# Optimization experiments

Hardware: AMD Instinct MI355X
Metric: run time of the kernel (lower is better)

## Reference

```python
import jax, jax.numpy as jnp
import numpy as np

CHAN = 128
IN_CHAN = 3
NB_OUT = 10
K = 2  # maxPoolKer


def affine_grid(theta, H, W):
    # theta: [C,2,3] -> grid [C,H,W,2], torch F.affine_grid align_corners=False
    xs = (2.0 * jnp.arange(W, dtype=jnp.float32) + 1.0) / W - 1.0
    ys = (2.0 * jnp.arange(H, dtype=jnp.float32) + 1.0) / H - 1.0
    gx, gy = jnp.meshgrid(xs, ys)  # [H,W]
    base = jnp.stack([gx, gy, jnp.ones_like(gx)], axis=-1)  # [H,W,3]
    return jnp.einsum('crk,hwk->chwr', theta, base)  # [...,0]=x, [...,1]=y


def grid_sample(img, grid):
    # img [M,H,W], grid [M,H,W,2]; bilinear, zeros padding, align_corners=False
    M, H, W = img.shape
    ix = ((grid[..., 0] + 1.0) * W - 1.0) * 0.5
    iy = ((grid[..., 1] + 1.0) * H - 1.0) * 0.5
    x0 = jnp.floor(ix)
    y0 = jnp.floor(iy)
    wx = ix - x0
    wy = iy - y0

    def tap(xi, yi):
        valid = (xi >= 0) & (xi <= W - 1) & (yi >= 0) & (yi <= H - 1)
        xc = jnp.clip(xi, 0, W - 1).astype(jnp.int32)
        yc = jnp.clip(yi, 0, H - 1).astype(jnp.int32)
        v = jax.vmap(lambda im, y, x: im[y, x])(img, yc, xc)
        return jnp.where(valid, v, 0.0)

    v00 = tap(x0, y0)
    v01 = tap(x0 + 1.0, y0)
    v10 = tap(x0, y0 + 1.0)
    v11 = tap(x0 + 1.0, y0 + 1.0)
    return (1.0 - wy) * ((1.0 - wx) * v00 + wx * v01) + wy * ((1.0 - wx) * v10 + wx * v11)


def geom_layer(x, geo, lin, box):
    # x [B,Ci,H,W]; lin [C,Ci]; geo,box [C,2,3]
    B, Ci, H, W = x.shape
    C = lin.shape[0]
    y = jnp.einsum('ci,bihw->bchw', lin, x)  # channel linear combine
    grid = affine_grid(geo, H, W)            # [C,H,W,2], shared across batch
    samp = jax.vmap(lambda yb: grid_sample(yb, grid))(y)  # [B,C,H,W]
    bgrid = affine_grid(box, H, W)
    boxm = grid_sample(jnp.ones((C, H, W), samp.dtype), bgrid)  # BoxPool mask
    return samp * boxm[None]


def maxpool_g(x, k):
    # MaxPool2d_G: depthwise box-filter conv -> argmax -> gather window from padded x
    B, C, H, W = x.shape
    ch, cw = H // k, W // k
    ker = jnp.ones((1, 1, ch, cw), x.dtype) / (ch + cw)
    xr = x.reshape(B * C, 1, H, W)
    conv = jax.lax.conv_general_dilated(
        xr, ker, (1, 1), [(ch // 2, ch // 2), (cw // 2, cw // 2)])
    conv = conv[:, :, :H, :W].reshape(B, C, H * W)
    argm = jnp.argmax(conv, axis=-1)
    r = argm // H  # original code uses origImgSize[0]; assumes square H==W
    c = argm % W
    padH, padW = H + H // k, W + W // k
    top = padH // 2 - H // 2
    left = padW // 2 - W // 2
    padded = jnp.zeros((B, C, padH, padW), x.dtype).at[:, :, top:top + H, left:left + W].set(x)
    r2 = r + H // (2 * k)
    c2 = c + W // (2 * k)
    ri = r2[..., None] + (jnp.arange(ch) - ch // 2)  # [B,C,ch]
    ci = c2[..., None] + (jnp.arange(cw) - cw // 2)  # [B,C,cw]
    gat = jax.vmap(jax.vmap(lambda p, rr, cc: p[rr[:, None], cc[None, :]]))(padded, ri, ci)
    return gat  # [B,C,ch,cw]


def setup_inputs() -> dict:
    key = jax.random.key(0)
    ks = jax.random.split(key, 12)
    eye = jnp.eye(3, dtype=jnp.float32)[:2]  # [2,3]
    x = jax.random.normal(ks[0], (8, IN_CHAN, 64, 64), dtype=jnp.float32)
    geo0 = eye[None] + 0.1 * jax.random.normal(ks[1], (CHAN, 2, 3), dtype=jnp.float32)
    lin0 = jax.random.uniform(ks[2], (CHAN, IN_CHAN), dtype=jnp.float32)
    box0 = eye[None] + 0.1 * jax.random.normal(ks[3], (CHAN, 2, 3), dtype=jnp.float32)
    geos = eye[None, None] + 0.1 * jax.random.normal(ks[4], (3, CHAN, 2, 3), dtype=jnp.float32)
    lins = jax.random.uniform(ks[5], (3, CHAN, CHAN), dtype=jnp.float32)
    boxes = eye[None, None] + 0.1 * jax.random.normal(ks[6], (3, CHAN, 2, 3), dtype=jnp.float32)
    bound = 1.0 / np.sqrt(CHAN)
    dense_w = jax.random.uniform(ks[7], (NB_OUT, CHAN), dtype=jnp.float32, minval=-bound, maxval=bound)
    dense_b = jax.random.uniform(ks[8], (NB_OUT,), dtype=jnp.float32, minval=-bound, maxval=bound)
    return {"x": x, "geo0": geo0, "lin0": lin0, "box0": box0,
            "geos": geos, "lins": lins, "boxes": boxes,
            "dense_w": dense_w, "dense_b": dense_b}


def reference(x, geo0, lin0, box0, geos, lins, boxes, dense_w, dense_b):
    h = geom_layer(x, geo0, lin0, box0)            # inLay: [8,128,64,64]
    h = geom_layer(h, geos[0], lins[0], boxes[0])  # layer 0
    h = maxpool_g(h, K)                            # layer 1 (maxPoolPos=1): [8,128,32,32]
    h = geom_layer(h, geos[1], lins[1], boxes[1])  # layer 2
    h = geom_layer(h, geos[2], lins[2], boxes[2])  # layer 3
    feat = h
    pooled = feat.mean(axis=-1).mean(axis=-1)      # [B,C]
    out = pooled @ dense_w.T + dense_b             # [B,nbOut]
    return out, feat
```

## Files before the change

### kernel.cpp

```cpp
#include <hip/hip_runtime.h>

#define BB 8
#define CC 128

__device__ __forceinline__ float sample_pad(const float* __restrict__ pl, int stride,
                                            float WF, float ix, float iy) {
  ix = fminf(fmaxf(ix, -1.0f), WF);
  iy = fminf(fmaxf(iy, -1.0f), WF);
  float x0f = floorf(ix), y0f = floorf(iy);
  float wx = ix - x0f, wy = iy - y0f;
  int xi = (int)x0f + 1, yi = (int)y0f + 1;
  const float* p0 = pl + yi * stride + xi;
  float v00 = p0[0], v01 = p0[1], v10 = p0[stride], v11 = p0[stride + 1];
  return (1.0f - wy) * ((1.0f - wx) * v00 + wx * v01) +
         wy * ((1.0f - wx) * v10 + wx * v11);
}

__device__ __forceinline__ float box_mask(float bix, float biy, float WM1) {
  float bx0 = floorf(bix), by0 = floorf(biy);
  float bwx = bix - bx0, bwy = biy - by0;
  float mx = (((bx0 >= 0.0f) && (bx0 <= WM1)) ? (1.0f - bwx) : 0.0f) +
             (((bx0 >= -1.0f) && (bx0 <= WM1 - 1.0f)) ? bwx : 0.0f);
  float my = (((by0 >= 0.0f) && (by0 <= WM1)) ? (1.0f - bwy) : 0.0f) +
             (((by0 >= -1.0f) && (by0 <= WM1 - 1.0f)) ? bwy : 0.0f);
  return mx * my;
}

__global__ __launch_bounds__(256) void inlay_sample_kernel(
    const float* __restrict__ x, const float* __restrict__ lin,
    const float* __restrict__ geo, const float* __restrict__ box,
    const float* __restrict__ db, float* __restrict__ out,
    float* __restrict__ head) {
  const int H = 64, W = 64, HW = 4096;
  __shared__ float cp[67 * 68];
  int bc = blockIdx.x;
  int c = bc & (CC - 1);
  int b = bc >> 7;
  int tid = threadIdx.x;
  if (bc == 0 && tid < 80) head[tid] = db[tid % 10];
  const float* xb = x + (size_t)b * 3 * HW;

  float w0 = lin[c * 3 + 0], w1 = lin[c * 3 + 1], w2 = lin[c * 3 + 2];

  if (tid < 68) {
    cp[tid] = 0.0f; cp[65 * 68 + tid] = 0.0f; cp[66 * 68 + tid] = 0.0f;
  } else if (tid < 132) {
    int r = tid - 67;
    cp[r * 68 + 0] = 0.0f; cp[r * 68 + 65] = 0.0f; cp[r * 68 + 66] = 0.0f;
  }

#pragma unroll
  for (int k = 0; k < 4; ++k) {
    int i4 = tid + k * 256;
    int base = i4 * 4;
    float4 f0 = *reinterpret_cast<const float4*>(&xb[base]);
    float4 f1 = *reinterpret_cast<const float4*>(&xb[HW + base]);
    float4 f2 = *reinterpret_cast<const float4*>(&xb[2 * HW + base]);
    int h = i4 >> 4, w = (i4 & 15) * 4;
    float* d = &cp[(h + 1) * 68 + w + 1];
    d[0] = w0 * f0.x + w1 * f1.x + w2 * f2.x;
    d[1] = w0 * f0.y + w1 * f1.y + w2 * f2.y;
    d[2] = w0 * f0.z + w1 * f1.z + w2 * f2.z;
    d[3] = w0 * f0.w + w1 * f1.w + w2 * f2.w;
  }
  __syncthreads();

  const float* g = geo + c * 6;
  const float* bx = box + c * 6;
  float g0 = g[0], g1 = g[1], g2 = g[2], g3 = g[3], g4 = g[4], g5 = g[5];
  float b0 = bx[0], b1 = bx[1], b2 = bx[2], b3 = bx[3], b4 = bx[4], b5 = bx[5];
  float* o = out + ((size_t)b * CC + c) * HW;

#pragma unroll
  for (int k = 0; k < 16; ++k) {
    int px = tid + k * 256;
    int h = px >> 6, w = px & 63;
    float xs = (2.0f * w + 1.0f) / W - 1.0f;
    float ys = (2.0f * h + 1.0f) / H - 1.0f;
    float ix = ((g0 * xs + g1 * ys + g2 + 1.0f) * W - 1.0f) * 0.5f;
    float iy = ((g3 * xs + g4 * ys + g5 + 1.0f) * H - 1.0f) * 0.5f;
    float samp = sample_pad(cp, 68, 64.0f, ix, iy);
    float bix = ((b0 * xs + b1 * ys + b2 + 1.0f) * W - 1.0f) * 0.5f;
    float biy = ((b3 * xs + b4 * ys + b5 + 1.0f) * H - 1.0f) * 0.5f;
    o[px] = samp * box_mask(bix, biy, 63.0f);
  }
}

__global__ __launch_bounds__(256) void gemm64_kernel(
    const float* __restrict__ lin, const float* __restrict__ x,
    float* __restrict__ y, int HW) {
  const int Ci = 128;
  __shared__ __align__(16) float As[16][68];
  __shared__ __align__(16) float Bs[16][64];
  int b = blockIdx.z;
  const float* xb = x + (size_t)b * Ci * HW;
  float* yb = y + (size_t)b * CC * HW;
  int tid = threadIdx.x;
  int tx = tid & 15, ty = tid >> 4;
  int row0 = blockIdx.y * 64;
  int col0 = blockIdx.x * 64;
  int m = tid >> 2, kq = (tid & 3) * 4;
  int kk = tid >> 4, n4 = (tid & 15) * 4;
  float acc[4][4] = {};
  float4 ra = *reinterpret_cast<const float4*>(&lin[(row0 + m) * Ci + kq]);
  float4 rb = *reinterpret_cast<const float4*>(&xb[(size_t)kk * HW + col0 + n4]);
  for (int k0 = 0; k0 < 128; k0 += 16) {
    __syncthreads();
    As[kq + 0][m] = ra.x; As[kq + 1][m] = ra.y; As[kq + 2][m] = ra.z; As[kq + 3][m] = ra.w;
    *reinterpret_cast<float4*>(&Bs[kk][n4]) = rb;
    __syncthreads();
    if (k0 + 16 < 128) {
      ra = *reinterpret_cast<const float4*>(&lin[(row0 + m) * Ci + k0 + 16 + kq]);
      rb = *reinterpret_cast<const float4*>(&xb[(size_t)(k0 + 16 + kk) * HW + col0 + n4]);
    }
#pragma unroll
    for (int kki = 0; kki < 16; ++kki) {
      float4 a4 = *reinterpret_cast<const float4*>(&As[kki][ty * 4]);
      float4 b4 = *reinterpret_cast<const float4*>(&Bs[kki][tx * 4]);
      float a[4] = {a4.x, a4.y, a4.z, a4.w};
      float bv[4] = {b4.x, b4.y, b4.z, b4.w};
#pragma unroll
      for (int i = 0; i < 4; i++)
#pragma unroll
        for (int j = 0; j < 4; j++) acc[i][j] += a[i] * bv[j];
    }
  }
#pragma unroll
  for (int i = 0; i < 4; i++) {
    float* yr = yb + (size_t)(row0 + ty * 4 + i) * HW + col0 + tx * 4;
    *reinterpret_cast<float4*>(yr) = make_float4(acc[i][0], acc[i][1], acc[i][2], acc[i][3]);
  }
}

__global__ __launch_bounds__(1024, 4) void sampmax_kernel(
    const float* __restrict__ y, const float* __restrict__ geo,
    const float* __restrict__ box, float* __restrict__ out) {
  __shared__ __align__(16) float sp[64 * 68];
  __shared__ __align__(16) float arena[64 * 100];
  __shared__ float wv[16];
  __shared__ int wi[16];
  __shared__ int am_s;
  float* pl = arena;
  float* cb = arena;

  int bc = blockIdx.x;
  int c = bc & (CC - 1);
  int tid = threadIdx.x;

  if (tid < 68) {
    pl[tid] = 0.0f; pl[65 * 68 + tid] = 0.0f; pl[66 * 68 + tid] = 0.0f;
  } else if (tid < 132) {
    int r = tid - 67;
    pl[r * 68 + 0] = 0.0f; pl[r * 68 + 65] = 0.0f; pl[r * 68 + 66] = 0.0f;
  }
  {
    const float* plane = y + (size_t)bc * 4096;
    float4 f = *reinterpret_cast<const float4*>(&plane[tid * 4]);
    int h = tid >> 4, w = (tid & 15) * 4;
    float* d = &pl[(h + 1) * 68 + w + 1];
    d[0] = f.x; d[1] = f.y; d[2] = f.z; d[3] = f.w;
  }
  __syncthreads();

  {
    const float* g = geo + c * 6;
    const float* bx = box + c * 6;
    float g0 = g[0], g1 = g[1], g2 = g[2], g3 = g[3], g4 = g[4], g5 = g[5];
    float b0 = bx[0], b1 = bx[1], b2 = bx[2], b3 = bx[3], b4 = bx[4], b5 = bx[5];
#pragma unroll
    for (int k = 0; k < 4; ++k) {
      int px = tid + k * 1024;
      int h = px >> 6, w = px & 63;
      float xs = (2.0f * w + 1.0f) / 64.0f - 1.0f;
      float ys = (2.0f * h + 1.0f) / 64.0f - 1.0f;
      float ix = ((g0 * xs + g1 * ys + g2 + 1.0f) * 64.0f - 1.0f) * 0.5f;
      float iy = ((g3 * xs + g4 * ys + g5 + 1.0f) * 64.0f - 1.0f) * 0.5f;
      float samp = sample_pad(pl, 68, 64.0f, ix, iy);
      float bix = ((b0 * xs + b1 * ys + b2 + 1.0f) * 64.0f - 1.0f) * 0.5f;
      float biy = ((b3 * xs + b4 * ys + b5 + 1.0f) * 64.0f - 1.0f) * 0.5f;
      sp[h * 68 + w] = samp * box_mask(bix, biy, 63.0f);
    }
  }
  __syncthreads();

  if (tid < 256) {
    int strip = tid >> 4, w4 = (tid & 15) * 4;
    int h0 = strip * 4;
    float4 a = make_float4(0.f, 0.f, 0.f, 0.f);
    float4 keep0 = a, keep1 = a, keep2 = a;
#pragma unroll
    for (int j = 0; j < 32; ++j) {
      int r = h0 + j - 16;
      bool valid = (r >= 0) && (r < 64);
      int rc = valid ? r : 0;
      float4 f = *reinterpret_cast<const float4*>(&sp[rc * 68 + w4]);
      f.x = valid ? f.x : 0.0f; f.y = valid ? f.y : 0.0f;
      f.z = valid ? f.z : 0.0f; f.w = valid ? f.w : 0.0f;
      if (j == 0) keep0 = f;
      if (j == 1) keep1 = f;
      if (j == 2) keep2 = f;
      a.x += f.x; a.y += f.y; a.z += f.z; a.w += f.w;
    }
    *reinterpret_cast<float4*>(&cb[(h0 + 0) * 100 + 16 + w4]) = a;
#pragma unroll
    for (int j = 32; j < 35; ++j) {
      int r = h0 + j - 16;
      bool valid = (r < 64);
      int rc = valid ? r : 0;
      float4 f = *reinterpret_cast<const float4*>(&sp[rc * 68 + w4]);
      f.x = valid ? f.x : 0.0f; f.y = valid ? f.y : 0.0f;
      f.z = valid ? f.z : 0.0f; f.w = valid ? f.w : 0.0f;
      float4 kp = (j == 32) ? keep0 : ((j == 33) ? keep1 : keep2);
      a.x += f.x - kp.x; a.y += f.y - kp.y; a.z += f.z - kp.z; a.w += f.w - kp.w;
      *reinterpret_cast<float4*>(&cb[(h0 + j - 31) * 100 + 16 + w4]) = a;
    }
  } else if (tid < 768) {
    int l = tid - 256;
    int row = l >> 3, gq = l & 7;
    int base = row * 100 + ((gq < 4) ? gq * 4 : 80 + (gq - 4) * 4);
    *reinterpret_cast<float4*>(&cb[base]) = make_float4(0.f, 0.f, 0.f, 0.f);
  }
  __syncthreads();

  float best = -3.402823466e+38f;
  int bidx = 0x7fffffff;
  {
    int h = tid >> 4, w4 = (tid & 15) * 4;
    float s0 = 0.f, k0 = 0.f, k1 = 0.f, k2 = 0.f;
#pragma unroll
    for (int q = 0; q < 8; ++q) {
      float4 f = *reinterpret_cast<const float4*>(&cb[h * 100 + w4 + 4 * q]);
      if (q == 0) { k0 = f.x; k1 = f.y; k2 = f.z; }
      s0 += f.x; s0 += f.y; s0 += f.z; s0 += f.w;
    }
    float4 ft = *reinterpret_cast<const float4*>(&cb[h * 100 + w4 + 32]);
    float s1 = s0 - k0 + ft.x;
    float s2 = s1 - k1 + ft.y;
    float s3 = s2 - k2 + ft.z;
    float sv[4] = {s0, s1, s2, s3};
#pragma unroll
    for (int d = 0; d < 4; ++d) {
      int i = (h << 6) + w4 + d;
      if (sv[d] > best) { best = sv[d]; bidx = i; }
    }
  }
#pragma unroll
  for (int off = 32; off > 0; off >>= 1) {
    float v2 = __shfl_down(best, off);
    int i2 = __shfl_down(bidx, off);
    if (v2 > best || (v2 == best && i2 < bidx)) { best = v2; bidx = i2; }
  }
  if ((tid & 63) == 0) { wv[tid >> 6] = best; wi[tid >> 6] = bidx; }
  __syncthreads();
  if (tid == 0) {
    float bv = wv[0]; int bi = wi[0];
#pragma unroll
    for (int k = 1; k < 16; ++k)
      if (wv[k] > bv || (wv[k] == bv && wi[k] < bi)) { bv = wv[k]; bi = wi[k]; }
    am_s = bi;
  }
  __syncthreads();

  int am = am_s;
  int r = am >> 6, cx = am & 63;
  float* o = out + (size_t)bc * 1024;
  {
    int oi = tid >> 5, oj = tid & 31;
    int rr = r + oi - 16, cj = cx + oj - 16;
    bool v = (rr >= 0) && (rr < 64) && (cj >= 0) && (cj < 64);
    int rrc = v ? rr : 0, cjc = v ? cj : 0;
    o[tid] = v ? sp[rrc * 68 + cjc] : 0.0f;
  }
}

template <bool POOL>
__global__ __launch_bounds__(256) void fused32_kernel(
    const float* __restrict__ lin, const float* __restrict__ x,
    const float* __restrict__ geo, const float* __restrict__ box,
    float* __restrict__ out, const float* __restrict__ dw,
    float* __restrict__ head) {
  const int H = 32, W = 32, HW = 1024;
  __shared__ float pls[2][35 * 36];
  __shared__ float wred[8];
  __shared__ float wsum[2];
  int b = blockIdx.x & 7;
  int c0 = (blockIdx.x >> 3) * 2;
  int tid = threadIdx.x;
  const float* xb = x + (size_t)b * 128 * HW;
  const float* l0 = lin + (c0 + 0) * 128;
  const float* l1 = lin + (c0 + 1) * 128;
  int px4 = tid * 4;

  if (tid < 36) {
#pragma unroll
    for (int cch = 0; cch < 2; ++cch) {
      pls[cch][tid] = 0.0f;
      pls[cch][33 * 36 + tid] = 0.0f;
      pls[cch][34 * 36 + tid] = 0.0f;
    }
  } else if (tid < 68) {
    int r = tid - 35;
#pragma unroll
    for (int cch = 0; cch < 2; ++cch) {
      pls[cch][r * 36 + 0] = 0.0f;
      pls[cch][r * 36 + 33] = 0.0f;
      pls[cch][r * 36 + 34] = 0.0f;
      pls[cch][r * 36 + 35] = 0.0f;
    }
  }

  float4 acc0 = make_float4(0.f, 0.f, 0.f, 0.f);
  float4 acc1 = acc0;
#pragma unroll 8
  for (int k = 0; k < 128; ++k) {
    float4 xv = *reinterpret_cast<const float4*>(&xb[(size_t)k * HW + px4]);
    float s0 = l0[k], s1 = l1[k];
    acc0.x += s0 * xv.x; acc0.y += s0 * xv.y; acc0.z += s0 * xv.z; acc0.w += s0 * xv.w;
    acc1.x += s1 * xv.x; acc1.y += s1 * xv.y; acc1.z += s1 * xv.z; acc1.w += s1 * xv.w;
  }
  {
    int h = px4 >> 5, w = px4 & 31;
    float* d0 = &pls[0][(h + 1) * 36 + w + 1];
    d0[0] = acc0.x; d0[1] = acc0.y; d0[2] = acc0.z; d0[3] = acc0.w;
    float* d1 = &pls[1][(h + 1) * 36 + w + 1];
    d1[0] = acc1.x; d1[1] = acc1.y; d1[2] = acc1.z; d1[3] = acc1.w;
  }
  __syncthreads();

  float psum[2] = {0.f, 0.f};
#pragma unroll
  for (int c = 0; c < 2; ++c) {
    const float* g = geo + (c0 + c) * 6;
    const float* bxp = box + (c0 + c) * 6;
    float g0 = g[0], g1 = g[1], g2 = g[2], g3 = g[3], g4 = g[4], g5 = g[5];
    float b0 = bxp[0], b1 = bxp[1], b2 = bxp[2], b3 = bxp[3], b4 = bxp[4], b5 = bxp[5];
    float* o = out + ((size_t)b * CC + c0 + c) * HW;
    const float* pl = pls[c];
#pragma unroll
    for (int k = 0; k < 4; ++k) {
      int px = tid + k * 256;
      int h = px >> 5, w = px & 31;
      float xs = (2.0f * w + 1.0f) / W - 1.0f;
      float ys = (2.0f * h + 1.0f) / H - 1.0f;
      float ix = ((g0 * xs + g1 * ys + g2 + 1.0f) * W - 1.0f) * 0.5f;
      float iy = ((g3 * xs + g4 * ys + g5 + 1.0f) * H - 1.0f) * 0.5f;
      float samp = sample_pad(pl, 36, 32.0f, ix, iy);
      float bix = ((b0 * xs + b1 * ys + b2 + 1.0f) * W - 1.0f) * 0.5f;
      float biy = ((b3 * xs + b4 * ys + b5 + 1.0f) * H - 1.0f) * 0.5f;
      float res = samp * box_mask(bix, biy, 31.0f);
      o[px] = res;
      if (POOL) psum[c] += res;
    }
  }
  if (POOL) {
    int lane = tid & 63, wid = tid >> 6;
#pragma unroll
    for (int c = 0; c < 2; ++c) {
      float r = psum[c];
#pragma unroll
      for (int off = 32; off > 0; off >>= 1) r += __shfl_down(r, off);
      if (lane == 0) wred[c * 4 + wid] = r;
    }
    __syncthreads();
    if (tid < 2) {
      float t = wred[tid * 4] + wred[tid * 4 + 1] + wred[tid * 4 + 2] + wred[tid * 4 + 3];
      wsum[tid] = t * (1.0f / 1024.0f);
    }
    __syncthreads();
    if (tid < 10) {
      float s = wsum[0] * dw[tid * 128 + c0] + wsum[1] * dw[tid * 128 + c0 + 1];
      atomicAdd(&head[b * 10 + tid], s);
    }
  }
}

extern "C" void kernel_launch(void* const* d_in, const int* in_sizes, int n_in,
                              void* d_out, int out_size, void* d_ws, size_t ws_size,
                              hipStream_t stream) {
  const float* x     = (const float*)d_in[0];
  const float* geo0  = (const float*)d_in[1];
  const float* lin0  = (const float*)d_in[2];
  const float* box0  = (const float*)d_in[3];
  const float* geos  = (const float*)d_in[4];
  const float* lins  = (const float*)d_in[5];
  const float* boxes = (const float*)d_in[6];
  const float* dw    = (const float*)d_in[7];
  const float* db    = (const float*)d_in[8];

  float* out  = (float*)d_out;
  float* feat = out + 80;
  float* ws   = (float*)d_ws;
  float* ws0  = ws;
  float* ws1  = ws + 4194304;

  inlay_sample_kernel<<<dim3(BB * CC), 256, 0, stream>>>(x, lin0, geo0, box0, db, ws1, out);
  gemm64_kernel<<<dim3(64, 2, BB), 256, 0, stream>>>(lins, ws1, ws0, 4096);
  sampmax_kernel<<<dim3(BB * CC), 1024, 0, stream>>>(ws0, geos, boxes, ws1);
  fused32_kernel<false><<<dim3(512), 256, 0, stream>>>(lins + 16384, ws1, geos + 768, boxes + 768, ws0, nullptr, nullptr);
  fused32_kernel<true><<<dim3(512), 256, 0, stream>>>(lins + 32768, ws0, geos + 1536, boxes + 1536, feat, dw, out);
}
```

Before: 157.5 us.

## Split 32x32 layers into tiled GEMM plus sampling kernels; shrink sampmax blocks

```diff
diff --git a/kernel.cpp b/kernel.cpp
--- a/kernel.cpp
+++ b/kernel.cpp
@@ -132,13 +132,13 @@
   }
 }
 
-__global__ __launch_bounds__(1024, 4) void sampmax_kernel(
+__global__ __launch_bounds__(256) void sampmax_kernel(
     const float* __restrict__ y, const float* __restrict__ geo,
     const float* __restrict__ box, float* __restrict__ out) {
   __shared__ __align__(16) float sp[64 * 68];
-  __shared__ __align__(16) float arena[64 * 100];
-  __shared__ float wv[16];
-  __shared__ int wi[16];
+  __shared__ __align__(16) float arena[67 * 68];
+  __shared__ float wv[4];
+  __shared__ int wi[4];
   __shared__ int am_s;
   float* pl = arena;
   float* cb = arena;
@@ -155,10 +155,14 @@
   }
   {
     const float* plane = y + (size_t)bc * 4096;
-    float4 f = *reinterpret_cast<const float4*>(&plane[tid * 4]);
-    int h = tid >> 4, w = (tid & 15) * 4;
-    float* d = &pl[(h + 1) * 68 + w + 1];
-    d[0] = f.x; d[1] = f.y; d[2] = f.z; d[3] = f.w;
+#pragma unroll
+    for (int k = 0; k < 4; ++k) {
+      int i4 = tid + k * 256;
+      float4 f = *reinterpret_cast<const float4*>(&plane[i4 * 4]);
+      int h = i4 >> 4, w = (i4 & 15) * 4;
+      float* d = &pl[(h + 1) * 68 + w + 1];
+      d[0] = f.x; d[1] = f.y; d[2] = f.z; d[3] = f.w;
+    }
   }
   __syncthreads();
 
@@ -168,8 +172,8 @@
     float g0 = g[0], g1 = g[1], g2 = g[2], g3 = g[3], g4 = g[4], g5 = g[5];
     float b0 = bx[0], b1 = bx[1], b2 = bx[2], b3 = bx[3], b4 = bx[4], b5 = bx[5];
 #pragma unroll
-    for (int k = 0; k < 4; ++k) {
-      int px = tid + k * 1024;
+    for (int k = 0; k < 16; ++k) {
+      int px = tid + k * 256;
       int h = px >> 6, w = px & 63;
       float xs = (2.0f * w + 1.0f) / 64.0f - 1.0f;
       float ys = (2.0f * h + 1.0f) / 64.0f - 1.0f;
@@ -183,7 +187,7 @@
   }
   __syncthreads();
 
-  if (tid < 256) {
+  {
     int strip = tid >> 4, w4 = (tid & 15) * 4;
     int h0 = strip * 4;
     float4 a = make_float4(0.f, 0.f, 0.f, 0.f);
@@ -201,7 +205,7 @@
       if (j == 2) keep2 = f;
       a.x += f.x; a.y += f.y; a.z += f.z; a.w += f.w;
     }
-    *reinterpret_cast<float4*>(&cb[(h0 + 0) * 100 + 16 + w4]) = a;
+    *reinterpret_cast<float4*>(&cb[(h0 + 0) * 68 + w4]) = a;
 #pragma unroll
     for (int j = 32; j < 35; ++j) {
       int r = h0 + j - 16;
@@ -212,31 +216,40 @@
       f.z = valid ? f.z : 0.0f; f.w = valid ? f.w : 0.0f;
       float4 kp = (j == 32) ? keep0 : ((j == 33) ? keep1 : keep2);
       a.x += f.x - kp.x; a.y += f.y - kp.y; a.z += f.z - kp.z; a.w += f.w - kp.w;
-      *reinterpret_cast<float4*>(&cb[(h0 + j - 31) * 100 + 16 + w4]) = a;
-    }
-  } else if (tid < 768) {
-    int l = tid - 256;
-    int row = l >> 3, gq = l & 7;
-    int base = row * 100 + ((gq < 4) ? gq * 4 : 80 + (gq - 4) * 4);
-    *reinterpret_cast<float4*>(&cb[base]) = make_float4(0.f, 0.f, 0.f, 0.f);
+      *reinterpret_cast<float4*>(&cb[(h0 + j - 31) * 68 + w4]) = a;
+    }
   }
   __syncthreads();
 
   float best = -3.402823466e+38f;
   int bidx = 0x7fffffff;
-  {
-    int h = tid >> 4, w4 = (tid & 15) * 4;
+#pragma unroll
+  for (int hh = 0; hh < 4; ++hh) {
+    int h = (tid >> 4) + hh * 16;
+    int w4 = (tid & 15) * 4;
     float s0 = 0.f, k0 = 0.f, k1 = 0.f, k2 = 0.f;
 #pragma unroll
     for (int q = 0; q < 8; ++q) {
-      float4 f = *reinterpret_cast<const float4*>(&cb[h * 100 + w4 + 4 * q]);
+      int u0 = w4 - 16 + 4 * q;
+      bool ok = (u0 >= 0) && (u0 <= 60);
+      int uc = ok ? u0 : 0;
+      float4 f = *reinterpret_cast<const float4*>(&cb[h * 68 + uc]);
+      f.x = ok ? f.x : 0.0f; f.y = ok ? f.y : 0.0f;
+      f.z = ok ? f.z : 0.0f; f.w = ok ? f.w : 0.0f;
       if (q == 0) { k0 = f.x; k1 = f.y; k2 = f.z; }
       s0 += f.x; s0 += f.y; s0 += f.z; s0 += f.w;
     }
-    float4 ft = *reinterpret_cast<const float4*>(&cb[h * 100 + w4 + 32]);
-    float s1 = s0 - k0 + ft.x;
-    float s2 = s1 - k1 + ft.y;
-    float s3 = s2 - k2 + ft.z;
+    float ftx = 0.f, fty = 0.f, ftz = 0.f;
+    {
+      int u0 = w4 + 16;
+      bool ok = (u0 <= 60);
+      int uc = ok ? u0 : 0;
+      float4 f = *reinterpret_cast<const float4*>(&cb[h * 68 + uc]);
+      ftx = ok ? f.x : 0.0f; fty = ok ? f.y : 0.0f; ftz = ok ? f.z : 0.0f;
+    }
+    float s1 = s0 - k0 + ftx;
+    float s2 = s1 - k1 + fty;
+    float s3 = s2 - k2 + ftz;
     float sv[4] = {s0, s1, s2, s3};
 #pragma unroll
     for (int d = 0; d < 4; ++d) {
@@ -255,7 +268,7 @@
   if (tid == 0) {
     float bv = wv[0]; int bi = wi[0];
 #pragma unroll
-    for (int k = 1; k < 16; ++k)
+    for (int k = 1; k < 4; ++k)
       if (wv[k] > bv || (wv[k] == bv && wi[k] < bi)) { bv = wv[k]; bi = wi[k]; }
     am_s = bi;
   }
@@ -264,112 +277,119 @@
   int am = am_s;
   int r = am >> 6, cx = am & 63;
   float* o = out + (size_t)bc * 1024;
-  {
-    int oi = tid >> 5, oj = tid & 31;
+#pragma unroll
+  for (int k = 0; k < 4; ++k) {
+    int idx = tid + k * 256;
+    int oi = idx >> 5, oj = idx & 31;
     int rr = r + oi - 16, cj = cx + oj - 16;
     bool v = (rr >= 0) && (rr < 64) && (cj >= 0) && (cj < 64);
     int rrc = v ? rr : 0, cjc = v ? cj : 0;
-    o[tid] = v ? sp[rrc * 68 + cjc] : 0.0f;
+    o[idx] = v ? sp[rrc * 68 + cjc] : 0.0f;
+  }
+}
+
+__global__ __launch_bounds__(256) void gemm32_kernel(
+    const float* __restrict__ lin, const float* __restrict__ x,
+    float* __restrict__ y) {
+  const int Ci = 128, HW = 1024;
+  __shared__ __align__(16) float As[16][36];
+  __shared__ __align__(16) float Bs[16][64];
+  int b = blockIdx.z;
+  const float* xb = x + (size_t)b * Ci * HW;
+  float* yb = y + (size_t)b * CC * HW;
+  int tid = threadIdx.x;
+  int tx = tid & 15, ty = tid >> 4;
+  int row0 = blockIdx.y * 32;
+  int col0 = blockIdx.x * 64;
+  int m = tid >> 2, kq = (tid & 3) * 4;
+  int kk = tid >> 4, n4 = (tid & 15) * 4;
+  float acc[2][4] = {};
+  float4 ra = make_float4(0.f, 0.f, 0.f, 0.f);
+  if (tid < 128) ra = *reinterpret_cast<const float4*>(&lin[(row0 + m) * Ci + kq]);
+  float4 rb = *reinterpret_cast<const float4*>(&xb[(size_t)kk * HW + col0 + n4]);
+  for (int k0 = 0; k0 < 128; k0 += 16) {
+    __syncthreads();
+    if (tid < 128) { As[kq + 0][m] = ra.x; As[kq + 1][m] = ra.y; As[kq + 2][m] = ra.z; As[kq + 3][m] = ra.w; }
+    *reinterpret_cast<float4*>(&Bs[kk][n4]) = rb;
+    __syncthreads();
+    if (k0 + 16 < 128) {
+      if (tid < 128) ra = *reinterpret_cast<const float4*>(&lin[(row0 + m) * Ci + k0 + 16 + kq]);
+      rb = *reinterpret_cast<const float4*>(&xb[(size_t)(k0 + 16 + kk) * HW + col0 + n4]);
+    }
+#pragma unroll
+    for (int kki = 0; kki < 16; ++kki) {
+      float a0 = As[kki][ty * 2], a1 = As[kki][ty * 2 + 1];
+      float4 b4 = *reinterpret_cast<const float4*>(&Bs[kki][tx * 4]);
+      acc[0][0] += a0 * b4.x; acc[0][1] += a0 * b4.y; acc[0][2] += a0 * b4.z; acc[0][3] += a0 * b4.w;
+      acc[1][0] += a1 * b4.x; acc[1][1] += a1 * b4.y; acc[1][2] += a1 * b4.z; acc[1][3] += a1 * b4.w;
+    }
+  }
+#pragma unroll
+  for (int i = 0; i < 2; i++) {
+    float* yr = yb + (size_t)(row0 + ty * 2 + i) * HW + col0 + tx * 4;
+    *reinterpret_cast<float4*>(yr) = make_float4(acc[i][0], acc[i][1], acc[i][2], acc[i][3]);
   }
 }
 
 template <bool POOL>
-__global__ __launch_bounds__(256) void fused32_kernel(
-    const float* __restrict__ lin, const float* __restrict__ x,
-    const float* __restrict__ geo, const float* __restrict__ box,
-    float* __restrict__ out, const float* __restrict__ dw,
-    float* __restrict__ head) {
-  const int H = 32, W = 32, HW = 1024;
-  __shared__ float pls[2][35 * 36];
-  __shared__ float wred[8];
-  __shared__ float wsum[2];
-  int b = blockIdx.x & 7;
-  int c0 = (blockIdx.x >> 3) * 2;
+__global__ __launch_bounds__(256) void sample32_kernel(
+    const float* __restrict__ y, const float* __restrict__ geo,
+    const float* __restrict__ box, float* __restrict__ out,
+    const float* __restrict__ dw, float* __restrict__ head) {
+  const int W = 32, HW = 1024;
+  __shared__ float pl[35 * 36];
+  __shared__ float wred[4];
+  int bc = blockIdx.x;
+  int c = bc & (CC - 1);
+  int b = bc >> 7;
   int tid = threadIdx.x;
-  const float* xb = x + (size_t)b * 128 * HW;
-  const float* l0 = lin + (c0 + 0) * 128;
-  const float* l1 = lin + (c0 + 1) * 128;
-  int px4 = tid * 4;
 
   if (tid < 36) {
-#pragma unroll
-    for (int cch = 0; cch < 2; ++cch) {
-      pls[cch][tid] = 0.0f;
-      pls[cch][33 * 36 + tid] = 0.0f;
-      pls[cch][34 * 36 + tid] = 0.0f;
-    }
+    pl[tid] = 0.0f; pl[33 * 36 + tid] = 0.0f; pl[34 * 36 + tid] = 0.0f;
   } else if (tid < 68) {
     int r = tid - 35;
-#pragma unroll
-    for (int cch = 0; cch < 2; ++cch) {
-      pls[cch][r * 36 + 0] = 0.0f;
-      pls[cch][r * 36 + 33] = 0.0f;
-      pls[cch][r * 36 + 34] = 0.0f;
-      pls[cch][r * 36 + 35] = 0.0f;
-    }
-  }
-
-  float4 acc0 = make_float4(0.f, 0.f, 0.f, 0.f);
-  float4 acc1 = acc0;
-#pragma unroll 8
-  for (int k = 0; k < 128; ++k) {
-    float4 xv = *reinterpret_cast<const float4*>(&xb[(size_t)k * HW + px4]);
-    float s0 = l0[k], s1 = l1[k];
-    acc0.x += s0 * xv.x; acc0.y += s0 * xv.y; acc0.z += s0 * xv.z; acc0.w += s0 * xv.w;
-    acc1.x += s1 * xv.x; acc1.y += s1 * xv.y; acc1.z += s1 * xv.z; acc1.w += s1 * xv.w;
+    pl[r * 36 + 0] = 0.0f; pl[r * 36 + 33] = 0.0f; pl[r * 36 + 34] = 0.0f; pl[r * 36 + 35] = 0.0f;
   }
   {
-    int h = px4 >> 5, w = px4 & 31;
-    float* d0 = &pls[0][(h + 1) * 36 + w + 1];
-    d0[0] = acc0.x; d0[1] = acc0.y; d0[2] = acc0.z; d0[3] = acc0.w;
-    float* d1 = &pls[1][(h + 1) * 36 + w + 1];
-    d1[0] = acc1.x; d1[1] = acc1.y; d1[2] = acc1.z; d1[3] = acc1.w;
-  }
-  __syncthreads();
-
-  float psum[2] = {0.f, 0.f};
-#pragma unroll
-  for (int c = 0; c < 2; ++c) {
-    const float* g = geo + (c0 + c) * 6;
-    const float* bxp = box + (c0 + c) * 6;
-    float g0 = g[0], g1 = g[1], g2 = g[2], g3 = g[3], g4 = g[4], g5 = g[5];
-    float b0 = bxp[0], b1 = bxp[1], b2 = bxp[2], b3 = bxp[3], b4 = bxp[4], b5 = bxp[5];
-    float* o = out + ((size_t)b * CC + c0 + c) * HW;
-    const float* pl = pls[c];
-#pragma unroll
-    for (int k = 0; k < 4; ++k) {
-      int px = tid + k * 256;
-      int h = px >> 5, w = px & 31;
-      float xs = (2.0f * w + 1.0f) / W - 1.0f;
-      float ys = (2.0f * h + 1.0f) / H - 1.0f;
-      float ix = ((g0 * xs + g1 * ys + g2 + 1.0f) * W - 1.0f) * 0.5f;
-      float iy = ((g3 * xs + g4 * ys + g5 + 1.0f) * H - 1.0f) * 0.5f;
-      float samp = sample_pad(pl, 36, 32.0f, ix, iy);
-      float bix = ((b0 * xs + b1 * ys + b2 + 1.0f) * W - 1.0f) * 0.5f;
-      float biy = ((b3 * xs + b4 * ys + b5 + 1.0f) * H - 1.0f) * 0.5f;
-      float res = samp * box_mask(bix, biy, 31.0f);
-      o[px] = res;
-      if (POOL) psum[c] += res;
-    }
+    const float* plane = y + (size_t)bc * HW;
+    float4 f = *reinterpret_cast<const float4*>(&plane[tid * 4]);
+    int h = tid >> 3, w = (tid & 7) * 4;
+    float* d = &pl[(h + 1) * 36 + w + 1];
+    d[0] = f.x; d[1] = f.y; d[2] = f.z; d[3] = f.w;
+  }
+  __syncthreads();
+
+  const float* g = geo + c * 6;
+  const float* bxp = box + c * 6;
+  float g0 = g[0], g1 = g[1], g2 = g[2], g3 = g[3], g4 = g[4], g5 = g[5];
+  float b0 = bxp[0], b1 = bxp[1], b2 = bxp[2], b3 = bxp[3], b4 = bxp[4], b5 = bxp[5];
+  float* o = out + (size_t)bc * HW;
+  float psum = 0.f;
+#pragma unroll
+  for (int k = 0; k < 4; ++k) {
+    int px = tid + k * 256;
+    int h = px >> 5, w = px & 31;
+    float xs = (2.0f * w + 1.0f) / W - 1.0f;
+    float ys = (2.0f * h + 1.0f) / W - 1.0f;
+    float ix = ((g0 * xs + g1 * ys + g2 + 1.0f) * W - 1.0f) * 0.5f;
+    float iy = ((g3 * xs + g4 * ys + g5 + 1.0f) * W - 1.0f) * 0.5f;
+    float samp = sample_pad(pl, 36, 32.0f, ix, iy);
+    float bix = ((b0 * xs + b1 * ys + b2 + 1.0f) * W - 1.0f) * 0.5f;
+    float biy = ((b3 * xs + b4 * ys + b5 + 1.0f) * W - 1.0f) * 0.5f;
+    float res = samp * box_mask(bix, biy, 31.0f);
+    o[px] = res;
+    if (POOL) psum += res;
   }
   if (POOL) {
     int lane = tid & 63, wid = tid >> 6;
-#pragma unroll
-    for (int c = 0; c < 2; ++c) {
-      float r = psum[c];
-#pragma unroll
-      for (int off = 32; off > 0; off >>= 1) r += __shfl_down(r, off);
-      if (lane == 0) wred[c * 4 + wid] = r;
-    }
-    __syncthreads();
-    if (tid < 2) {
-      float t = wred[tid * 4] + wred[tid * 4 + 1] + wred[tid * 4 + 2] + wred[tid * 4 + 3];
-      wsum[tid] = t * (1.0f / 1024.0f);
-    }
+    float r = psum;
+#pragma unroll
+    for (int off = 32; off > 0; off >>= 1) r += __shfl_down(r, off);
+    if (lane == 0) wred[wid] = r;
     __syncthreads();
     if (tid < 10) {
-      float s = wsum[0] * dw[tid * 128 + c0] + wsum[1] * dw[tid * 128 + c0 + 1];
-      atomicAdd(&head[b * 10 + tid], s);
+      float t = (wred[0] + wred[1] + wred[2] + wred[3]) * (1.0f / 1024.0f);
+      atomicAdd(&head[b * 10 + tid], t * dw[tid * 128 + c]);
     }
   }
 }
@@ -392,10 +412,13 @@
   float* ws   = (float*)d_ws;
   float* ws0  = ws;
   float* ws1  = ws + 4194304;
+  float* ws2  = ws + 8388608;
 
   inlay_sample_kernel<<<dim3(BB * CC), 256, 0, stream>>>(x, lin0, geo0, box0, db, ws1, out);
   gemm64_kernel<<<dim3(64, 2, BB), 256, 0, stream>>>(lins, ws1, ws0, 4096);
-  sampmax_kernel<<<dim3(BB * CC), 1024, 0, stream>>>(ws0, geos, boxes, ws1);
-  fused32_kernel<false><<<dim3(512), 256, 0, stream>>>(lins + 16384, ws1, geos + 768, boxes + 768, ws0, nullptr, nullptr);
-  fused32_kernel<true><<<dim3(512), 256, 0, stream>>>(lins + 32768, ws0, geos + 1536, boxes + 1536, feat, dw, out);
-}
+  sampmax_kernel<<<dim3(BB * CC), 256, 0, stream>>>(ws0, geos, boxes, ws1);
+  gemm32_kernel<<<dim3(16, 4, BB), 256, 0, stream>>>(lins + 16384, ws1, ws2);
+  sample32_kernel<false><<<dim3(BB * CC), 256, 0, stream>>>(ws2, geos + 768, boxes + 768, ws0, nullptr, nullptr);
+  gemm32_kernel<<<dim3(16, 4, BB), 256, 0, stream>>>(lins + 32768, ws0, ws2);
+  sample32_kernel<true><<<dim3(BB * CC), 256, 0, stream>>>(ws2, geos + 1536, boxes + 1536, feat, dw, out);
+}
```

Measured after the change: 151.7 us. 1.04x faster.
